# Optimization experiments

Hardware: AMD Instinct MI355X
Metric: run time of the kernel (lower is better)

Reference implementation:

```python
import jax, jax.numpy as jnp
import numpy as np

N_LAYERS = 2
D_MODEL = 1024
D_STATE = 16
D_CONV = 4
EXPAND = 2
D_INNER = EXPAND * D_MODEL
DT_RANK = (D_MODEL + 15) // 16  # ceil(d_model/16) = 64
B, T = 2, 1024
LN_EPS = 1e-5


def setup_inputs() -> dict:
    key = jax.random.key(0)
    ks = jax.random.split(key, 12)
    L = N_LAYERS
    x = jax.random.normal(ks[0], (B, T, D_MODEL), jnp.float32)
    in_proj_w = 0.02 * jax.random.normal(ks[1], (L, 2 * D_INNER, D_MODEL), jnp.float32)
    conv_w = 0.2 * jax.random.normal(ks[2], (L, D_INNER, D_CONV), jnp.float32)
    conv_b = jnp.zeros((L, D_INNER), jnp.float32)
    x_proj_w = 0.02 * jax.random.normal(ks[3], (L, DT_RANK + 2 * D_STATE, D_INNER), jnp.float32)
    dt_proj_w = 0.02 * jax.random.normal(ks[4], (L, D_INNER, DT_RANK), jnp.float32)
    dt_proj_b = jnp.full((L, D_INNER), -4.6, jnp.float32)  # softplus^-1(~0.01)
    # S4D-real init: A_log[d, n] = log(n+1)
    A_log = jnp.broadcast_to(jnp.log(jnp.arange(1, D_STATE + 1, dtype=jnp.float32)), (L, D_INNER, D_STATE))
    Dskip = jnp.ones((L, D_INNER), jnp.float32)
    out_proj_w = 0.02 * jax.random.normal(ks[5], (L, D_MODEL, D_INNER), jnp.float32)
    ln_w = jnp.ones((L, D_MODEL), jnp.float32)
    ln_b = jnp.zeros((L, D_MODEL), jnp.float32)
    return {"x": x, "in_proj_w": in_proj_w, "conv_w": conv_w, "conv_b": conv_b,
            "x_proj_w": x_proj_w, "dt_proj_w": dt_proj_w, "dt_proj_b": dt_proj_b,
            "A_log": A_log, "Dskip": Dskip, "out_proj_w": out_proj_w,
            "ln_w": ln_w, "ln_b": ln_b}


def _layer_norm(x, w, b):
    mu = jnp.mean(x, axis=-1, keepdims=True)
    xc = x - mu
    var = jnp.mean(xc * xc, axis=-1, keepdims=True)
    return xc * jax.lax.rsqrt(var + LN_EPS) * w + b


def _mamba_layer(x, in_w, cw, cb, xp_w, dt_w, dt_b, A_log, Dskip, out_w):
    # x: [B, T, D_MODEL]
    xz = jnp.einsum('btd,ed->bte', x, in_w)  # [B,T,2*D_INNER]
    xc, z = jnp.split(xz, 2, axis=-1)
    # causal depthwise conv1d, kernel D_CONV
    pad = D_CONV - 1
    xpad = jnp.pad(xc, ((0, 0), (pad, 0), (0, 0)))
    Tlen = xc.shape[1]
    conv = sum(xpad[:, k:k + Tlen, :] * cw[:, k] for k in range(D_CONV)) + cb
    u = jax.nn.silu(conv)  # [B,T,D_INNER]
    x_dbl = jnp.einsum('btd,ed->bte', u, xp_w)
    dt, Bm, Cm = jnp.split(x_dbl, [DT_RANK, DT_RANK + D_STATE], axis=-1)
    dt = jax.nn.softplus(jnp.einsum('btr,dr->btd', dt, dt_w) + dt_b)  # [B,T,D_INNER]
    A = -jnp.exp(A_log)  # [D_INNER, D_STATE]

    def step(h, inp):
        dt_t, B_t, C_t, u_t = inp  # [B,d_in], [B,N], [B,N], [B,d_in]
        dA = jnp.exp(dt_t[:, :, None] * A)                      # [B,d_in,N]
        h = dA * h + (dt_t * u_t)[:, :, None] * B_t[:, None, :]  # [B,d_in,N]
        y = jnp.einsum('bdn,bn->bd', h, C_t)
        return h, y

    h0 = jnp.zeros((x.shape[0], D_INNER, D_STATE), x.dtype)
    _, ys = jax.lax.scan(step, h0, (dt.transpose(1, 0, 2), Bm.transpose(1, 0, 2),
                                    Cm.transpose(1, 0, 2), u.transpose(1, 0, 2)))
    y = ys.transpose(1, 0, 2) + u * Dskip  # [B,T,D_INNER]
    y = y * jax.nn.silu(z)
    return jnp.einsum('bti,oi->bto', y, out_w)  # [B,T,D_MODEL]


def reference(x, in_proj_w, conv_w, conv_b, x_proj_w, dt_proj_w, dt_proj_b,
              A_log, Dskip, out_proj_w, ln_w, ln_b):
    for l in range(N_LAYERS):
        residual = x
        h = _mamba_layer(x, in_proj_w[l], conv_w[l], conv_b[l], x_proj_w[l],
                         dt_proj_w[l], dt_proj_b[l], A_log[l], Dskip[l], out_proj_w[l])
        h = _layer_norm(h, ln_w[l], ln_b[l])
        x = h + residual  # dropout=0 -> Identity
    return x
```

## Files before the change

### kernel.cpp

```cpp
#include <hip/hip_runtime.h>

constexpr int BN = 2;
constexpr int TN = 1024;
constexpr int DM = 1024;
constexpr int DI = 2048;
constexpr int DS = 16;
constexpr int RK = 64;
constexpr int XD = 96;
constexpr int XDP = 128;
constexpr int MROWS = BN * TN;
constexpr int NC = 32;
constexpr int CL = 32;
constexpr int XPZ = 8;
constexpr int OPZ = 4;

using f32x4  = __attribute__((ext_vector_type(4))) float;
using bf16x8 = __attribute__((ext_vector_type(8))) short;

__device__ inline short f2b(float f) {
  union { float f; unsigned u; } v; v.f = f;
  unsigned r = (v.u + 0x7FFFu + ((v.u >> 16) & 1u)) >> 16;
  return (short)r;
}
__device__ inline float b2f(short s) {
  union { unsigned u; float f; } v; v.u = ((unsigned)(unsigned short)s) << 16;
  return v.f;
}
__device__ inline float fexp(float x) { return __builtin_amdgcn_exp2f(x * 1.4426950408889634f); }
__device__ inline float fsilu(float x) { return x * __builtin_amdgcn_rcpf(1.f + fexp(-x)); }
__device__ inline float fsoftplus(float v) { return (v > 15.f) ? v : __logf(1.f + __expf(v)); }

__device__ inline void gl_lds16(const void* g, void* l) {
  __builtin_amdgcn_global_load_lds((const __attribute__((address_space(1))) void*)g,
                                   (__attribute__((address_space(3))) void*)l, 16, 0, 0);
}

__global__ __launch_bounds__(256) void f2bf_k(const float* __restrict__ in,
    short* __restrict__ out, int n4) {
  int i = blockIdx.x * 256 + threadIdx.x;
  if (i >= n4) return;
  float4 v = ((const float4*)in)[i];
  short4 s; s.x = f2b(v.x); s.y = f2b(v.y); s.z = f2b(v.z); s.w = f2b(v.w);
  ((short4*)out)[i] = s;
}

__global__ __launch_bounds__(256) void xpw_pad_k(const float* __restrict__ in,
    short* __restrict__ out) {
  int i = blockIdx.x * 256 + threadIdx.x;
  int c4 = i & (DI / 4 - 1);
  int rl = i >> 9;
  int r = rl & (XDP - 1), l = rl >> 7;
  short4 s;
  if (r < XD) {
    float4 v = ((const float4*)(in + ((long)l * XD + r) * DI))[c4];
    s.x = f2b(v.x); s.y = f2b(v.y); s.z = f2b(v.z); s.w = f2b(v.w);
  } else { s.x = s.y = s.z = s.w = 0; }
  ((short4*)(out + ((long)l * XDP + r) * DI))[c4] = s;
}

template<int MODE, int KS>
__global__ __launch_bounds__(256) void gemm_mfma(const short* __restrict__ A,
    const short* __restrict__ Bw, float* __restrict__ Cf, short* __restrict__ Cb,
    int M, int N, int K, int lda, int ldb, int ldc,
    const float* __restrict__ bias, int ksplit) {
  __shared__ alignas(16) short As[2][128 * 32];
  __shared__ alignas(16) short Bs[2][128 * 32];
  const int tid = threadIdx.x;
  const int wid = tid >> 6, lane = tid & 63;
  const int row0 = blockIdx.y * 128, col0 = blockIdx.x * 128;
  const int wr = (wid >> 1) * 64, wc = (wid & 1) * 64;
  const int srow = tid >> 2;
  const int scol = (tid & 3) * 8;
  f32x4 acc[4][4] = {};
  const int kbeg = KS ? blockIdx.z * ksplit : 0;
  const int kend = KS ? kbeg + ksplit : K;

  auto stage = [&](int buf, int k0) {
#pragma unroll
    for (int r = 0; r < 2; ++r) {
      gl_lds16(A  + (long)(row0 + r * 64 + srow) * lda + k0 + scol,
               (short*)((char*)As[buf] + r * 4096 + wid * 1024));
      gl_lds16(Bw + (long)(col0 + r * 64 + srow) * ldb + k0 + scol,
               (short*)((char*)Bs[buf] + r * 4096 + wid * 1024));
    }
  };

  stage(0, kbeg);
  int buf = 0;
  for (int k0 = kbeg; k0 < kend; k0 += 32, buf ^= 1) {
    if (k0 + 32 < kend) {
      stage(buf ^ 1, k0 + 32);
      asm volatile("s_waitcnt vmcnt(4)" ::: "memory");
    } else {
      asm volatile("s_waitcnt vmcnt(0)" ::: "memory");
    }
    __builtin_amdgcn_s_barrier();
    bf16x8 af[4], bv[4];
#pragma unroll
    for (int i = 0; i < 4; ++i)
      af[i] = *(const bf16x8*)(As[buf] + (wr + i * 16 + (lane & 15)) * 32 + (lane >> 4) * 8);
#pragma unroll
    for (int j = 0; j < 4; ++j)
      bv[j] = *(const bf16x8*)(Bs[buf] + (wc + j * 16 + (lane & 15)) * 32 + (lane >> 4) * 8);
#pragma unroll
    for (int i = 0; i < 4; ++i)
#pragma unroll
      for (int j = 0; j < 4; ++j)
        acc[i][j] = __builtin_amdgcn_mfma_f32_16x16x32_bf16(af[i], bv[j], acc[i][j], 0, 0, 0);
    __builtin_amdgcn_s_barrier();
  }
  const long zbase = KS ? (long)blockIdx.z * M * ldc : 0;
#pragma unroll
  for (int i = 0; i < 4; ++i) {
#pragma unroll
    for (int j = 0; j < 4; ++j) {
      int gcol = col0 + wc + j * 16 + (lane & 15);
#pragma unroll
      for (int r = 0; r < 4; ++r) {
        int grow = row0 + wr + i * 16 + (lane >> 4) * 4 + r;
        if (MODE == 1) Cb[(long)grow * ldc + gcol] = f2b(acc[i][j][r]);
        else if (MODE == 2) {
          float v = acc[i][j][r] + bias[gcol];
          Cf[(long)grow * ldc + gcol] = fsoftplus(v);
        } else Cf[zbase + (long)grow * ldc + gcol] = acc[i][j][r];
      }
    }
  }
}

__global__ __launch_bounds__(256) void reduce_xp(const float* __restrict__ part,
    float* __restrict__ out, short* __restrict__ outb) {
  int i = blockIdx.x * 256 + threadIdx.x;
  const int n = MROWS * XDP;
  float s = 0.f;
#pragma unroll
  for (int z = 0; z < XPZ; ++z) s += part[(long)z * n + i];
  out[i] = s;
  outb[i] = f2b(s);
}

__global__ __launch_bounds__(256) void conv_silu(const short* __restrict__ xz,
    const float* __restrict__ cw, const float* __restrict__ cb,
    short* __restrict__ ubf) {
  int idx = blockIdx.x * 256 + threadIdx.x;
  int d = idx & (DI - 1);
  int bt = idx >> 11;
  int t = bt & (TN - 1);
  long rowb = (long)(bt - t);
  float acc = cb[d];
#pragma unroll
  for (int k = 0; k < 4; ++k) {
    int ts = t - 3 + k;
    if (ts >= 0) acc = fmaf(b2f(xz[(rowb + ts) * (2 * DI) + d]), cw[d * 4 + k], acc);
  }
  ubf[idx] = f2b(fsilu(acc));
}

__global__ __launch_bounds__(256) void scan_p1(const float* __restrict__ dt,
    const short* __restrict__ u, const float* __restrict__ xdbl,
    const float* __restrict__ A_log, float* __restrict__ hloc,
    float* __restrict__ prodb) {
  int tid = threadIdx.x;
  int bid = blockIdx.x;
  int dblk = bid & 7, cb_ = bid >> 3, b = cb_ & 1, c = cb_ >> 1;
  int d = dblk * 256 + tid;
  float Av[16];
  {
    const float4* Ap = (const float4*)(A_log + (long)d * DS);
#pragma unroll
    for (int q = 0; q < 4; ++q) {
      float4 a = Ap[q];
      Av[4*q+0] = -__expf(a.x); Av[4*q+1] = -__expf(a.y);
      Av[4*q+2] = -__expf(a.z); Av[4*q+3] = -__expf(a.w);
    }
  }
  float h[16] = {};
  float sdt = 0.f;
  long row = (long)b * TN + c * CL;
  for (int t = 0; t < CL; ++t) {
    long rw = row + t;
    float dtv = dt[rw * DI + d];
    float uv  = b2f(u[rw * DI + d]);
    float du = dtv * uv;
    sdt += dtv;
    const float4* Bp = (const float4*)(xdbl + rw * XDP + RK);
#pragma unroll
    for (int q = 0; q < 4; ++q) {
      float4 Bv = Bp[q];
      h[4*q+0] = fmaf(fexp(dtv * Av[4*q+0]), h[4*q+0], du * Bv.x);
      h[4*q+1] = fmaf(fexp(dtv * Av[4*q+1]), h[4*q+1], du * Bv.y);
      h[4*q+2] = fmaf(fexp(dtv * Av[4*q+2]), h[4*q+2], du * Bv.z);
      h[4*q+3] = fmaf(fexp(dtv * Av[4*q+3]), h[4*q+3], du * Bv.w);
    }
  }
  long o = (((long)c * BN + b) * DI + d) * DS;
  float4* hp = (float4*)(hloc + o);
  float4* pp = (float4*)(prodb + o);
#pragma unroll
  for (int q = 0; q < 4; ++q) {
    float4 hv; hv.x = h[4*q]; hv.y = h[4*q+1]; hv.z = h[4*q+2]; hv.w = h[4*q+3];
    hp[q] = hv;
    float4 pv;
    pv.x = fexp(sdt * Av[4*q+0]); pv.y = fexp(sdt * Av[4*q+1]);
    pv.z = fexp(sdt * Av[4*q+2]); pv.w = fexp(sdt * Av[4*q+3]);
    pp[q] = pv;
  }
}

__global__ __launch_bounds__(256) void scan_p2(const float* __restrict__ hloc,
    const float* __restrict__ prodb, float* __restrict__ h0) {
  long idx = blockIdx.x * 256 + threadIdx.x;
  float carry = 0.f;
  for (int c = 0; c < NC; ++c) {
    long o = (long)c * (BN * DI * DS) + idx;
    h0[o] = carry;
    carry = fmaf(prodb[o], carry, hloc[o]);
  }
}

__global__ __launch_bounds__(256) void scan_p3(const float* __restrict__ dt,
    const short* __restrict__ u, const float* __restrict__ xdbl,
    const short* __restrict__ xz, const float* __restrict__ A_log,
    const float* __restrict__ Dskip, const float* __restrict__ h0,
    short* __restrict__ ybf) {
  int tid = threadIdx.x;
  int bid = blockIdx.x;
  int dblk = bid & 7, cb_ = bid >> 3, b = cb_ & 1, c = cb_ >> 1;
  int d = dblk * 256 + tid;
  float Av[16];
  {
    const float4* Ap = (const float4*)(A_log + (long)d * DS);
#pragma unroll
    for (int q = 0; q < 4; ++q) {
      float4 a = Ap[q];
      Av[4*q+0] = -__expf(a.x); Av[4*q+1] = -__expf(a.y);
      Av[4*q+2] = -__expf(a.z); Av[4*q+3] = -__expf(a.w);
    }
  }
  float Dval = Dskip[d];
  float h[16];
  {
    const float4* hp = (const float4*)(h0 + (((long)c * BN + b) * DI + d) * DS);
#pragma unroll
    for (int q = 0; q < 4; ++q) {
      float4 hv = hp[q];
      h[4*q] = hv.x; h[4*q+1] = hv.y; h[4*q+2] = hv.z; h[4*q+3] = hv.w;
    }
  }
  long row = (long)b * TN + c * CL;
  for (int t = 0; t < CL; ++t) {
    long rw = row + t;
    float dtv = dt[rw * DI + d];
    float uv  = b2f(u[rw * DI + d]);
    float du = dtv * uv;
    const float4* Bp = (const float4*)(xdbl + rw * XDP + RK);
    const float4* Cp = (const float4*)(xdbl + rw * XDP + RK + DS);
    float y = 0.f;
#pragma unroll
    for (int q = 0; q < 4; ++q) {
      float4 Bv = Bp[q];
      float4 Cv = Cp[q];
      h[4*q+0] = fmaf(fexp(dtv * Av[4*q+0]), h[4*q+0], du * Bv.x);
      h[4*q+1] = fmaf(fexp(dtv * Av[4*q+1]), h[4*q+1], du * Bv.y);
      h[4*q+2] = fmaf(fexp(dtv * Av[4*q+2]), h[4*q+2], du * Bv.z);
      h[4*q+3] = fmaf(fexp(dtv * Av[4*q+3]), h[4*q+3], du * Bv.w);
      y = fmaf(h[4*q+0], Cv.x, y);
      y = fmaf(h[4*q+1], Cv.y, y);
      y = fmaf(h[4*q+2], Cv.z, y);
      y = fmaf(h[4*q+3], Cv.w, y);
    }
    float zv = b2f(xz[rw * (2 * DI) + DI + d]);
    ybf[rw * DI + d] = f2b((y + uv * Dval) * fsilu(zv));
  }
}

__global__ __launch_bounds__(256) void ln_res(const float* __restrict__ hp,
    const float* __restrict__ resid, const float* __restrict__ w,
    const float* __restrict__ bb, float* __restrict__ out, short* __restrict__ ob) {
  int row = blockIdx.x;
  int tid = threadIdx.x;
  const long n = (long)MROWS * DM;
  const long base = (long)row * DM;
  float4 v;
  {
    float4 p0 = ((const float4*)(hp + base))[tid];
    float4 p1 = ((const float4*)(hp + n + base))[tid];
    float4 p2 = ((const float4*)(hp + 2 * n + base))[tid];
    float4 p3 = ((const float4*)(hp + 3 * n + base))[tid];
    v.x = p0.x + p1.x + p2.x + p3.x;
    v.y = p0.y + p1.y + p2.y + p3.y;
    v.z = p0.z + p1.z + p2.z + p3.z;
    v.w = p0.w + p1.w + p2.w + p3.w;
  }
  __shared__ float sm[256];
  float s = v.x + v.y + v.z + v.w;
  sm[tid] = s; __syncthreads();
  for (int st = 128; st > 0; st >>= 1) { if (tid < st) sm[tid] += sm[tid + st]; __syncthreads(); }
  float mean = sm[0] * (1.f / DM);
  __syncthreads();
  float4 c;
  c.x = v.x - mean; c.y = v.y - mean; c.z = v.z - mean; c.w = v.w - mean;
  float s2 = c.x * c.x + c.y * c.y + c.z * c.z + c.w * c.w;
  sm[tid] = s2; __syncthreads();
  for (int st = 128; st > 0; st >>= 1) { if (tid < st) sm[tid] += sm[tid + st]; __syncthreads(); }
  float inv = rsqrtf(sm[0] * (1.f / DM) + 1e-5f);
  const float4 rv = ((const float4*)(resid + base))[tid];
  const float4 wv = ((const float4*)w)[tid];
  const float4 bv = ((const float4*)bb)[tid];
  float4 ov;
  ov.x = c.x * inv * wv.x + bv.x + rv.x;
  ov.y = c.y * inv * wv.y + bv.y + rv.y;
  ov.z = c.z * inv * wv.z + bv.z + rv.z;
  ov.w = c.w * inv * wv.w + bv.w + rv.w;
  ((float4*)(out + base))[tid] = ov;
  if (ob) {
    short4 sv; sv.x = f2b(ov.x); sv.y = f2b(ov.y); sv.z = f2b(ov.z); sv.w = f2b(ov.w);
    *(short4*)(ob + base + tid * 4) = sv;
  }
}

extern "C" void kernel_launch(void* const* d_in, const int* in_sizes, int n_in,
                              void* d_out, int out_size, void* d_ws, size_t ws_size,
                              hipStream_t stream) {
  const float* x     = (const float*)d_in[0];
  const float* inw   = (const float*)d_in[1];
  const float* convw = (const float*)d_in[2];
  const float* convb = (const float*)d_in[3];
  const float* xpw   = (const float*)d_in[4];
  const float* dtw   = (const float*)d_in[5];
  const float* dtbi  = (const float*)d_in[6];
  const float* alog  = (const float*)d_in[7];
  const float* dsk   = (const float*)d_in[8];
  const float* outw  = (const float*)d_in[9];
  const float* lnw   = (const float*)d_in[10];
  const float* lnb   = (const float*)d_in[11];
  float* outp = (float*)d_out;

  char* w = (char*)d_ws; size_t off = 0;
  auto alloc = [&](size_t bytes) { void* p = w + off; off += (bytes + 255) & ~255ULL; return p; };
  short* inw_bf  = (short*)alloc((size_t)2 * 2 * DI * DM * 2);
  short* outw_bf = (short*)alloc((size_t)2 * DM * DI * 2);
  short* dtw_bf  = (short*)alloc((size_t)2 * DI * RK * 2);
  short* xpw_bf  = (short*)alloc((size_t)2 * XDP * DI * 2);
  short* abuf    = (short*)alloc((size_t)MROWS * DI * 2);
  short* xzbf    = (short*)alloc((size_t)MROWS * 2 * DI * 2);
  short* ubf     = (short*)alloc((size_t)MROWS * DI * 2);
  float* arena   = (float*)alloc((size_t)OPZ * MROWS * DM * 4);
  float* xpart   = arena;
  float* hloc    = arena;
  float* prodb   = arena +     (size_t)NC * BN * DI * DS;
  float* h0      = arena + 2 * (size_t)NC * BN * DI * DS;
  float* hb4     = arena;
  float* xdb     = (float*)alloc((size_t)MROWS * XDP * 4);
  short* xdbf    = (short*)alloc((size_t)MROWS * XDP * 2);
  float* dtb     = (float*)alloc((size_t)MROWS * DI * 4);
  float* xcur    = (float*)alloc((size_t)MROWS * DM * 4);

  f2bf_k<<<(MROWS * DM / 4 + 255) / 256, 256, 0, stream>>>(x, abuf, MROWS * DM / 4);
  f2bf_k<<<(2 * 2 * DI * DM / 4 + 255) / 256, 256, 0, stream>>>(inw, inw_bf, 2 * 2 * DI * DM / 4);
  f2bf_k<<<(2 * DM * DI / 4 + 255) / 256, 256, 0, stream>>>(outw, outw_bf, 2 * DM * DI / 4);
  f2bf_k<<<(2 * DI * RK / 4 + 255) / 256, 256, 0, stream>>>(dtw, dtw_bf, 2 * DI * RK / 4);
  xpw_pad_k<<<(2 * XDP * DI / 4 + 255) / 256, 256, 0, stream>>>(xpw, xpw_bf);

  const float* lin = x;
  for (int l = 0; l < 2; ++l) {
    gemm_mfma<1, 0><<<dim3((2 * DI) / 128, MROWS / 128), 256, 0, stream>>>(
        abuf, inw_bf + (size_t)l * 2 * DI * DM, nullptr, xzbf,
        MROWS, 2 * DI, DM, DM, DM, 2 * DI, nullptr, 0);

    conv_silu<<<(MROWS * DI) / 256, 256, 0, stream>>>(
        xzbf, convw + (size_t)l * DI * 4, convb + (size_t)l * DI, ubf);

    gemm_mfma<0, 1><<<dim3(1, MROWS / 128, XPZ), 256, 0, stream>>>(
        ubf, xpw_bf + (size_t)l * XDP * DI, xpart, nullptr,
        MROWS, XDP, DI, DI, DI, XDP, nullptr, DI / XPZ);
    reduce_xp<<<(MROWS * XDP) / 256, 256, 0, stream>>>(xpart, xdb, xdbf);

    gemm_mfma<2, 0><<<dim3(DI / 128, MROWS / 128), 256, 0, stream>>>(
        xdbf, dtw_bf + (size_t)l * DI * RK, dtb, nullptr,
        MROWS, DI, RK, XDP, RK, DI, dtbi + (size_t)l * DI, 0);

    scan_p1<<<NC * BN * (DI / 256), 256, 0, stream>>>(dtb, ubf, xdb,
        alog + (size_t)l * DI * DS, hloc, prodb);
    scan_p2<<<(BN * DI * DS) / 256, 256, 0, stream>>>(hloc, prodb, h0);
    scan_p3<<<NC * BN * (DI / 256), 256, 0, stream>>>(dtb, ubf, xdb, xzbf,
        alog + (size_t)l * DI * DS, dsk + (size_t)l * DI, h0, abuf);

    gemm_mfma<0, 1><<<dim3(DM / 128, MROWS / 128, OPZ), 256, 0, stream>>>(
        abuf, outw_bf + (size_t)l * DM * DI, hb4, nullptr,
        MROWS, DM, DI, DI, DI, DM, nullptr, DI / OPZ);

    float* lo = (l == 0) ? xcur : outp;
    short* lob = (l == 0) ? abuf : nullptr;
    ln_res<<<MROWS, 256, 0, stream>>>(hb4, lin,
        lnw + (size_t)l * DM, lnb + (size_t)l * DM, lo, lob);
    lin = xcur;
  }
}
```

Baseline: 321.9 us.

## Deepen GEMM K-tile to 64 with swizzled LDS, store dt in bf16, fuse prep kernels

The GEMM now stages 64-wide K tiles instead of 32, halving the number of barrier and loop iterations, and uses an XOR swizzle on LDS columns to avoid bank conflicts when reading MFMA fragments. The dt projection output is written as bf16 rather than fp32, halving the traffic the two scan kernels spend reading dt. The five weight and input conversion kernels are merged into one launch to cut launch overhead. The LDS footprint doubles, which may lower occupancy, and storing dt in bf16 loses precision in the scan.

Result: faster. 297.9 us (-7.5%).

```diff
diff --git a/kernel.cpp b/kernel.cpp
--- a/kernel.cpp
+++ b/kernel.cpp
@@ -35,27 +35,40 @@
                                    (__attribute__((address_space(3))) void*)l, 16, 0, 0);
 }
 
-__global__ __launch_bounds__(256) void f2bf_k(const float* __restrict__ in,
-    short* __restrict__ out, int n4) {
+constexpr int PR0 = MROWS * DM / 4;
+constexpr int PR1 = PR0 + 4 * DI * DM / 4;
+constexpr int PR2 = PR1 + 2 * DM * DI / 4;
+constexpr int PR3 = PR2 + 2 * DI * RK / 4;
+constexpr int PR4 = PR3 + 2 * XDP * DI / 4;
+__global__ __launch_bounds__(256) void prep_k(const float* __restrict__ x,
+    const float* __restrict__ inw, const float* __restrict__ outw,
+    const float* __restrict__ dtw, const float* __restrict__ xpw,
+    short* __restrict__ abuf, short* __restrict__ inw_bf,
+    short* __restrict__ outw_bf, short* __restrict__ dtw_bf,
+    short* __restrict__ xpw_bf) {
   int i = blockIdx.x * 256 + threadIdx.x;
-  if (i >= n4) return;
-  float4 v = ((const float4*)in)[i];
+  if (i >= PR4) return;
+  const float* src = nullptr; short* dst = nullptr; int j = i;
+  if (i < PR0)      { src = x;    dst = abuf;    }
+  else if (i < PR1) { j = i - PR0; src = inw;  dst = inw_bf;  }
+  else if (i < PR2) { j = i - PR1; src = outw; dst = outw_bf; }
+  else if (i < PR3) { j = i - PR2; src = dtw;  dst = dtw_bf;  }
+  else {
+    j = i - PR3;
+    int c4 = j & (DI / 4 - 1);
+    int rl = j >> 9;
+    int r = rl & (XDP - 1), l = rl >> 7;
+    short4 s;
+    if (r < XD) {
+      float4 v = ((const float4*)(xpw + ((long)l * XD + r) * DI))[c4];
+      s.x = f2b(v.x); s.y = f2b(v.y); s.z = f2b(v.z); s.w = f2b(v.w);
+    } else { s.x = s.y = s.z = s.w = 0; }
+    ((short4*)xpw_bf)[j] = s;
+    return;
+  }
+  float4 v = ((const float4*)src)[j];
   short4 s; s.x = f2b(v.x); s.y = f2b(v.y); s.z = f2b(v.z); s.w = f2b(v.w);
-  ((short4*)out)[i] = s;
-}
-
-__global__ __launch_bounds__(256) void xpw_pad_k(const float* __restrict__ in,
-    short* __restrict__ out) {
-  int i = blockIdx.x * 256 + threadIdx.x;
-  int c4 = i & (DI / 4 - 1);
-  int rl = i >> 9;
-  int r = rl & (XDP - 1), l = rl >> 7;
-  short4 s;
-  if (r < XD) {
-    float4 v = ((const float4*)(in + ((long)l * XD + r) * DI))[c4];
-    s.x = f2b(v.x); s.y = f2b(v.y); s.z = f2b(v.z); s.w = f2b(v.w);
-  } else { s.x = s.y = s.z = s.w = 0; }
-  ((short4*)(out + ((long)l * XDP + r) * DI))[c4] = s;
+  ((short4*)dst)[j] = s;
 }
 
 template<int MODE, int KS>
@@ -63,50 +76,55 @@
     const short* __restrict__ Bw, float* __restrict__ Cf, short* __restrict__ Cb,
     int M, int N, int K, int lda, int ldb, int ldc,
     const float* __restrict__ bias, int ksplit) {
-  __shared__ alignas(16) short As[2][128 * 32];
-  __shared__ alignas(16) short Bs[2][128 * 32];
+  __shared__ alignas(16) short As[2][128 * 64];
+  __shared__ alignas(16) short Bs[2][128 * 64];
   const int tid = threadIdx.x;
   const int wid = tid >> 6, lane = tid & 63;
   const int row0 = blockIdx.y * 128, col0 = blockIdx.x * 128;
   const int wr = (wid >> 1) * 64, wc = (wid & 1) * 64;
-  const int srow = tid >> 2;
-  const int scol = (tid & 3) * 8;
+  const int tr = tid >> 3;
+  const int tg = (tid & 7) ^ (tr & 7);
   f32x4 acc[4][4] = {};
   const int kbeg = KS ? blockIdx.z * ksplit : 0;
   const int kend = KS ? kbeg + ksplit : K;
 
   auto stage = [&](int buf, int k0) {
 #pragma unroll
-    for (int r = 0; r < 2; ++r) {
-      gl_lds16(A  + (long)(row0 + r * 64 + srow) * lda + k0 + scol,
-               (short*)((char*)As[buf] + r * 4096 + wid * 1024));
-      gl_lds16(Bw + (long)(col0 + r * 64 + srow) * ldb + k0 + scol,
-               (short*)((char*)Bs[buf] + r * 4096 + wid * 1024));
+    for (int r2 = 0; r2 < 4; ++r2) {
+      gl_lds16(A  + (long)(row0 + r2 * 32 + tr) * lda + k0 + tg * 8,
+               (short*)((char*)As[buf] + r2 * 4096 + tid * 16));
+      gl_lds16(Bw + (long)(col0 + r2 * 32 + tr) * ldb + k0 + tg * 8,
+               (short*)((char*)Bs[buf] + r2 * 4096 + tid * 16));
     }
   };
 
   stage(0, kbeg);
   int buf = 0;
-  for (int k0 = kbeg; k0 < kend; k0 += 32, buf ^= 1) {
-    if (k0 + 32 < kend) {
-      stage(buf ^ 1, k0 + 32);
-      asm volatile("s_waitcnt vmcnt(4)" ::: "memory");
+  for (int k0 = kbeg; k0 < kend; k0 += 64, buf ^= 1) {
+    if (k0 + 64 < kend) {
+      stage(buf ^ 1, k0 + 64);
+      asm volatile("s_waitcnt vmcnt(8)" ::: "memory");
     } else {
       asm volatile("s_waitcnt vmcnt(0)" ::: "memory");
     }
     __builtin_amdgcn_s_barrier();
-    bf16x8 af[4], bv[4];
-#pragma unroll
-    for (int i = 0; i < 4; ++i)
-      af[i] = *(const bf16x8*)(As[buf] + (wr + i * 16 + (lane & 15)) * 32 + (lane >> 4) * 8);
-#pragma unroll
-    for (int j = 0; j < 4; ++j)
-      bv[j] = *(const bf16x8*)(Bs[buf] + (wc + j * 16 + (lane & 15)) * 32 + (lane >> 4) * 8);
-#pragma unroll
-    for (int i = 0; i < 4; ++i)
-#pragma unroll
-      for (int j = 0; j < 4; ++j)
-        acc[i][j] = __builtin_amdgcn_mfma_f32_16x16x32_bf16(af[i], bv[j], acc[i][j], 0, 0, 0);
+    bf16x8 af[2][4], bv[2][4];
+#pragma unroll
+    for (int ks = 0; ks < 2; ++ks) {
+#pragma unroll
+      for (int i = 0; i < 4; ++i) {
+        int ca = ((ks * 4 + (lane >> 4)) ^ (lane & 7)) * 8;
+        af[ks][i] = *(const bf16x8*)(As[buf] + (wr + i * 16 + (lane & 15)) * 64 + ca);
+        bv[ks][i] = *(const bf16x8*)(Bs[buf] + (wc + i * 16 + (lane & 15)) * 64 + ca);
+      }
+    }
+#pragma unroll
+    for (int ks = 0; ks < 2; ++ks)
+#pragma unroll
+      for (int i = 0; i < 4; ++i)
+#pragma unroll
+        for (int j = 0; j < 4; ++j)
+          acc[i][j] = __builtin_amdgcn_mfma_f32_16x16x32_bf16(af[ks][i], bv[ks][j], acc[i][j], 0, 0, 0);
     __builtin_amdgcn_s_barrier();
   }
   const long zbase = KS ? (long)blockIdx.z * M * ldc : 0;
@@ -121,7 +139,7 @@
         if (MODE == 1) Cb[(long)grow * ldc + gcol] = f2b(acc[i][j][r]);
         else if (MODE == 2) {
           float v = acc[i][j][r] + bias[gcol];
-          Cf[(long)grow * ldc + gcol] = fsoftplus(v);
+          Cb[(long)grow * ldc + gcol] = f2b(fsoftplus(v));
         } else Cf[zbase + (long)grow * ldc + gcol] = acc[i][j][r];
       }
     }
@@ -156,7 +174,7 @@
   ubf[idx] = f2b(fsilu(acc));
 }
 
-__global__ __launch_bounds__(256) void scan_p1(const float* __restrict__ dt,
+__global__ __launch_bounds__(256) void scan_p1(const short* __restrict__ dt,
     const short* __restrict__ u, const float* __restrict__ xdbl,
     const float* __restrict__ A_log, float* __restrict__ hloc,
     float* __restrict__ prodb) {
@@ -179,7 +197,7 @@
   long row = (long)b * TN + c * CL;
   for (int t = 0; t < CL; ++t) {
     long rw = row + t;
-    float dtv = dt[rw * DI + d];
+    float dtv = b2f(dt[rw * DI + d]);
     float uv  = b2f(u[rw * DI + d]);
     float du = dtv * uv;
     sdt += dtv;
@@ -218,7 +236,7 @@
   }
 }
 
-__global__ __launch_bounds__(256) void scan_p3(const float* __restrict__ dt,
+__global__ __launch_bounds__(256) void scan_p3(const short* __restrict__ dt,
     const short* __restrict__ u, const float* __restrict__ xdbl,
     const short* __restrict__ xz, const float* __restrict__ A_log,
     const float* __restrict__ Dskip, const float* __restrict__ h0,
@@ -250,7 +268,7 @@
   long row = (long)b * TN + c * CL;
   for (int t = 0; t < CL; ++t) {
     long rw = row + t;
-    float dtv = dt[rw * DI + d];
+    float dtv = b2f(dt[rw * DI + d]);
     float uv  = b2f(u[rw * DI + d]);
     float du = dtv * uv;
     const float4* Bp = (const float4*)(xdbl + rw * XDP + RK);
@@ -353,14 +371,11 @@
   float* hb4     = arena;
   float* xdb     = (float*)alloc((size_t)MROWS * XDP * 4);
   short* xdbf    = (short*)alloc((size_t)MROWS * XDP * 2);
-  float* dtb     = (float*)alloc((size_t)MROWS * DI * 4);
+  short* dtb     = (short*)alloc((size_t)MROWS * DI * 2);
   float* xcur    = (float*)alloc((size_t)MROWS * DM * 4);
 
-  f2bf_k<<<(MROWS * DM / 4 + 255) / 256, 256, 0, stream>>>(x, abuf, MROWS * DM / 4);
-  f2bf_k<<<(2 * 2 * DI * DM / 4 + 255) / 256, 256, 0, stream>>>(inw, inw_bf, 2 * 2 * DI * DM / 4);
-  f2bf_k<<<(2 * DM * DI / 4 + 255) / 256, 256, 0, stream>>>(outw, outw_bf, 2 * DM * DI / 4);
-  f2bf_k<<<(2 * DI * RK / 4 + 255) / 256, 256, 0, stream>>>(dtw, dtw_bf, 2 * DI * RK / 4);
-  xpw_pad_k<<<(2 * XDP * DI / 4 + 255) / 256, 256, 0, stream>>>(xpw, xpw_bf);
+  prep_k<<<(PR4 + 255) / 256, 256, 0, stream>>>(x, inw, outw, dtw, xpw,
+      abuf, inw_bf, outw_bf, dtw_bf, xpw_bf);
 
   const float* lin = x;
   for (int l = 0; l < 2; ++l) {
@@ -377,7 +392,7 @@
     reduce_xp<<<(MROWS * XDP) / 256, 256, 0, stream>>>(xpart, xdb, xdbf);
 
     gemm_mfma<2, 0><<<dim3(DI / 128, MROWS / 128), 256, 0, stream>>>(
-        xdbf, dtw_bf + (size_t)l * DI * RK, dtb, nullptr,
+        xdbf, dtw_bf + (size_t)l * DI * RK, nullptr, dtb,
         MROWS, DI, RK, XDP, RK, DI, dtbi + (size_t)l * DI, 0);
 
     scan_p1<<<NC * BN * (DI / 256), 256, 0, stream>>>(dtb, ubf, xdb,
```
